# Kernel optimization log

Hardware: AMD Instinct MI355X
Metric: run time of the kernel (lower is better)

Reference implementation:

```python
import jax, jax.numpy as jnp
import numpy as np

N_NODES = 50000
N_EDGES = 800000
N_ENT = 500000
N_REL = 500
L = 2          # num_layers
H = 8          # head_num
D = 16         # per-head dim (hidden_dim // head_num)
HID = H * D    # 128
IN = 128       # in_ent_dim == in_rel_dim == hidden_dim
B = 64         # number of graphs in the batch
SLOPE = 0.2    # leaky-relu negative slope


def setup_inputs() -> dict:
    key = jax.random.key(0)
    ks = jax.random.split(key, 11)
    return {
        "ent_table": jax.random.normal(ks[0], (N_ENT, IN), jnp.float32) * 0.05,
        "rel_table": jax.random.normal(ks[1], (N_REL, IN), jnp.float32) * 0.05,
        "W_ent": jax.random.normal(ks[2], (L, IN, HID), jnp.float32) * 0.05,
        "W_rel": jax.random.normal(ks[3], (L, IN, HID), jnp.float32) * 0.05,
        "attn_l": jax.random.normal(ks[4], (L, H, D), jnp.float32) * 0.05,
        "attn_r": jax.random.normal(ks[5], (L, H, D), jnp.float32) * 0.05,
        "attn_e": jax.random.normal(ks[6], (L, H, D), jnp.float32) * 0.05,
        "ent_ids": jax.random.randint(ks[7], (N_NODES,), 0, N_ENT, jnp.int32),
        "rel_ids": jax.random.randint(ks[8], (N_EDGES,), 0, N_REL, jnp.int32),
        "src": jax.random.randint(ks[9], (N_EDGES,), 0, N_NODES, jnp.int32),
        "dst": jax.random.randint(ks[10], (N_EDGES,), 0, N_NODES, jnp.int32),
        # node-0 offset of each subgraph in the batched graph
        "graph_offsets": jnp.arange(B, dtype=jnp.int32) * (N_NODES // B),
    }


def _kge_layer(h, rel_f, src, dst, W_e, W_r, a_l, a_r, a_e):
    # GAT-style relation-aware message passing (KGELayer)
    feat = (h @ W_e).reshape(-1, H, D)        # [N,H,D]
    rfeat = (rel_f @ W_r).reshape(-1, H, D)   # [E,H,D]
    el = jnp.einsum('nhd,hd->nh', feat, a_l)  # src score
    er = jnp.einsum('nhd,hd->nh', feat, a_r)  # dst score
    ee = jnp.einsum('ehd,hd->eh', rfeat, a_e) # relation score
    e = jax.nn.leaky_relu(el[src] + er[dst] + ee, SLOPE)  # [E,H]
    # segment softmax over incoming edges of each dst node
    emax = jax.ops.segment_max(e, dst, num_segments=N_NODES)
    ex = jnp.exp(e - emax[dst])
    denom = jax.ops.segment_sum(ex, dst, num_segments=N_NODES)
    alpha = ex / denom[dst]                   # [E,H]
    msg = (feat[src] + rfeat) * alpha[:, :, None]  # [E,H,D]
    out = jax.ops.segment_sum(msg, dst, num_segments=N_NODES)  # [N,H,D]
    return out.reshape(-1, HID)


def reference(ent_table, rel_table, W_ent, W_rel, attn_l, attn_r, attn_e,
              ent_ids, rel_ids, src, dst, graph_offsets):
    h = ent_table[ent_ids]       # [N,IN]
    rel_f = rel_table[rel_ids]   # [E,IN]
    for l in range(L):
        h = _kge_layer(h, rel_f, src, dst, W_ent[l], W_rel[l],
                       attn_l[l], attn_r[l], attn_e[l])
    # CLS embedding: node 0 of each unbatched subgraph
    return h[graph_offsets]      # [B,HID]
```

## Files before the change

### kernel.cpp

```cpp
#include <hip/hip_runtime.h>
#include <hip/hip_bf16.h>


#define NN   50000
#define NE   800000
#define NR   500
#define HH   8
#define DD   16
#define HIDD 128
#define BB   64

#define GRIDS 1024
#define PER   784

#define MAXE2 16384
#define MAXS1 16448
#define MAXE1 262144
#define MAXS0 50000


__global__ void k_init(int* slot2, int* slot1, int* slot0, int* counters) {
    int i = blockIdx.x * blockDim.x + threadIdx.x;
    int stride = gridDim.x * blockDim.x;
    for (int n = i; n < NN; n += stride) { slot2[n] = -1; slot1[n] = -1; slot0[n] = -1; }
    if (i < 8) counters[i] = 0;
}

__global__ void k_seed(const int* goffs, int* slot2, int* slot1, int* nodesS1) {
    int i = threadIdx.x;
    if (i < BB) {
        int n = goffs[i];
        slot2[n] = i;
        slot1[n] = -2;
        nodesS1[i] = n;
    }
}

__global__ void k_scan(const int* __restrict__ src, const int* __restrict__ dst,
                       const int* __restrict__ slotHit, int* __restrict__ slotNew,
                       int* eseg, int* ecnt, int* nseg, int* ncnt) {
    __shared__ int cE, cN;
    if (threadIdx.x == 0) { cE = 0; cN = 0; }
    __syncthreads();
    int b = blockIdx.x;
    int lo = b * PER;
    int hi = lo + PER; if (hi > NE) hi = NE;
    int* es = eseg + (size_t)b * PER;
    int* ns = nseg + (size_t)b * PER;
    for (int e = lo + threadIdx.x; e < hi; e += blockDim.x) {
        int d = dst[e];
        if (slotHit[d] >= 0) {
            int pos = atomicAdd(&cE, 1);
            es[pos] = e;
            int s = src[e];
            if (atomicCAS(&slotNew[s], -1, -2) == -1) {
                int p = atomicAdd(&cN, 1);
                ns[p] = s;
            }
        }
    }
    __syncthreads();
    if (threadIdx.x == 0) { ecnt[b] = cE; ncnt[b] = cN; }
}

__device__ int block_scan_counts(const int* cnts, int nblk, int* bases, int offset) {
    __shared__ int part[256];
    __shared__ int total_sh;
    int t = threadIdx.x;
    int per = (nblk + 255) / 256;
    int s = 0;
    for (int j = 0; j < per; j++) { int i = t * per + j; if (i < nblk) s += cnts[i]; }
    part[t] = s;
    __syncthreads();
    for (int d = 1; d < 256; d <<= 1) {
        int v = (t >= d) ? part[t - d] : 0;
        __syncthreads();
        part[t] += v;
        __syncthreads();
    }
    int run = ((t == 0) ? 0 : part[t - 1]) + offset;
    for (int j = 0; j < per; j++) {
        int i = t * per + j;
        if (i < nblk) { bases[i] = run; run += cnts[i]; }
    }
    if (t == 255) total_sh = part[255];
    __syncthreads();
    return total_sh;
}

__global__ void k_prefix2(const int* ecnt2, const int* ncnt2, int* ebase2, int* nbase2,
                          int* counters, const int* nodesS1, int* slot1, int* slot0,
                          int* nodesS0) {
    int t = threadIdx.x;
    int totE = block_scan_counts(ecnt2, GRIDS, ebase2, 0);
    int totN = block_scan_counts(ncnt2, GRIDS, nbase2, BB);
    if (t == 0) {
        counters[2] = totE;
        counters[0] = BB + totN;
        counters[1] = BB + totN;
    }
    if (t < BB) {
        int n = nodesS1[t];
        slot1[n] = t;
        slot0[n] = t;
        nodesS0[t] = n;
    }
}

__global__ void k_compact2(const int* eseg2, const int* ecnt2, const int* ebase2,
                           const int* nseg2, const int* ncnt2, const int* nbase2,
                           int* e2list, int* nodesS1, int* slot1, int* slot0,
                           int* nodesS0, int* deg2) {
    int b = blockIdx.x, t = threadIdx.x;
    int ce = ecnt2[b], cn = ncnt2[b], be = ebase2[b], bn = nbase2[b];
    const int* es = eseg2 + (size_t)b * PER;
    const int* ns = nseg2 + (size_t)b * PER;
    for (int i = t; i < ce; i += blockDim.x) {
        int g = be + i; if (g < MAXE2) e2list[g] = es[i];
    }
    for (int i = t; i < cn; i += blockDim.x) {
        int idx = bn + i;
        if (idx < MAXS1) {
            int n = ns[i];
            nodesS1[idx] = n;
            slot1[n] = idx;
            slot0[n] = idx;
            nodesS0[idx] = n;
        }
    }
    if (b == 0) { for (int i = t; i < BB; i += blockDim.x) deg2[i] = 0; }
}

__global__ void k_prefix1(const int* ecnt1, const int* ncnt1, int* ebase1, int* nbase1,
                          int* counters) {
    int t = threadIdx.x;
    int s0 = counters[1];
    int totE = block_scan_counts(ecnt1, GRIDS, ebase1, 0);
    int totN = block_scan_counts(ncnt1, GRIDS, nbase1, s0);
    if (t == 0) {
        counters[3] = totE;
        counters[1] = s0 + totN;
    }
}

__global__ void k_compact1(const int* eseg1, const int* ecnt1, const int* ebase1,
                           const int* nseg1, const int* ncnt1, const int* nbase1,
                           int* e1list, int* slot0, int* nodesS0,
                           int* deg1, const int* counters) {
    int b = blockIdx.x, t = threadIdx.x;
    int ce = ecnt1[b], cn = ncnt1[b], be = ebase1[b], bn = nbase1[b];
    const int* es = eseg1 + (size_t)b * PER;
    const int* ns = nseg1 + (size_t)b * PER;
    for (int i = t; i < ce; i += blockDim.x) {
        int g = be + i; if (g < MAXE1) e1list[g] = es[i];
    }
    for (int i = t; i < cn; i += blockDim.x) {
        int idx = bn + i;
        if (idx < MAXS0) {
            int n = ns[i];
            slot0[n] = idx;
            nodesS0[idx] = n;
        }
    }
    int cnt1 = counters[0]; if (cnt1 > MAXS1) cnt1 = MAXS1;
    for (int i = b * blockDim.x + t; i < cnt1; i += gridDim.x * blockDim.x) deg1[i] = 0;
}

__global__ void k_hist(const int* e2list, const int* e1list, const int* counters,
                       const int* dst, const int* slot2, const int* slot1,
                       int* deg2, int* deg1) {
    int i = blockIdx.x * blockDim.x + threadIdx.x;
    int stride = gridDim.x * blockDim.x;
    int c2 = counters[2]; if (c2 > MAXE2) c2 = MAXE2;
    int c1 = counters[3]; if (c1 > MAXE1) c1 = MAXE1;
    for (int k = i; k < c2; k += stride) atomicAdd(&deg2[slot2[dst[e2list[k]]]], 1);
    for (int k = i; k < c1; k += stride) atomicAdd(&deg1[slot1[dst[e1list[k]]]], 1);
}

__device__ void excl_scan_glob(const int* deg, int n, int* rp) {
    __shared__ int part[256];
    int t = threadIdx.x;
    int per = (n + 255) / 256;
    int s = 0;
    for (int j = 0; j < per; j++) { int i = t * per + j; if (i < n) s += deg[i]; }
    part[t] = s;
    __syncthreads();
    for (int d = 1; d < 256; d <<= 1) {
        int v = (t >= d) ? part[t - d] : 0;
        __syncthreads();
        part[t] += v;
        __syncthreads();
    }
    int run = (t == 0) ? 0 : part[t - 1];
    for (int j = 0; j < per; j++) {
        int i = t * per + j;
        if (i < n) { rp[i] = run; run += deg[i]; }
    }
    if (t == 255) rp[n] = part[255];
    __syncthreads();
}

__global__ void k_rowptr(const int* deg2, const int* deg1, const int* counters,
                         int* rp2, int* rp1, int* cur2, int* cur1) {
    int t = threadIdx.x;
    int cnt1 = counters[0]; if (cnt1 > MAXS1) cnt1 = MAXS1;
    excl_scan_glob(deg2, BB, rp2);
    excl_scan_glob(deg1, cnt1, rp1);
    for (int i = t; i < BB; i += blockDim.x) cur2[i] = rp2[i];
    for (int i = t; i < cnt1; i += blockDim.x) cur1[i] = rp1[i];
}

__global__ void k_scatter(const int* e2list, const int* e1list, const int* counters,
                          const int* dst, const int* slot2, const int* slot1,
                          int* cur2, int* cur1, int* csr2, int* csr1) {
    int i = blockIdx.x * blockDim.x + threadIdx.x;
    int stride = gridDim.x * blockDim.x;
    int c2 = counters[2]; if (c2 > MAXE2) c2 = MAXE2;
    int c1 = counters[3]; if (c1 > MAXE1) c1 = MAXE1;
    for (int k = i; k < c2; k += stride) {
        int e = e2list[k];
        int pos = atomicAdd(&cur2[slot2[dst[e]]], 1);
        if (pos < MAXE2) csr2[pos] = e;
    }
    for (int k = i; k < c1; k += stride) {
        int e = e1list[k];
        int pos = atomicAdd(&cur1[slot1[dst[e]]], 1);
        if (pos < MAXE1) csr1[pos] = e;
    }
}

#define FT 8
__global__ void k_relfeat0(const float* rel_table, const float* __restrict__ W_rel,
                           const float* attn_e, float* rproj, float* ee,
                           const int* nodesS0, const int* counters, const int* ent_ids,
                           const float* __restrict__ ent_table,
                           const float* __restrict__ W_ent,
                           const float* __restrict__ attn_l,
                           const float* __restrict__ attn_r,
                           float* feat0, float* el0, float* er0) {
    __shared__ float rows[FT][HIDD];
    int t = threadIdx.x;
    if (blockIdx.x < 2 * NR) {
        int l = blockIdx.x / NR, r = blockIdx.x % NR;
        rows[0][t] = rel_table[r * HIDD + t];
        __syncthreads();
        const float* W = W_rel + l * HIDD * HIDD;
        float acc = 0.f;
        for (int j = 0; j < HIDD; j++) acc += rows[0][j] * W[j * HIDD + t];
        rproj[(l * NR + r) * HIDD + t] = acc;
        rows[1][t] = acc;
        __syncthreads();
        if (t < HH) {
            float s = 0.f;
            for (int d = 0; d < DD; d++)
                s += rows[1][t * DD + d] * attn_e[(l * HH + t) * DD + d];
            ee[(l * NR + r) * HH + t] = s;
        }
        return;
    }
    int cnt = counters[1]; if (cnt > MAXS0) cnt = MAXS0;
    int tile0 = blockIdx.x - 2 * NR;
    int tstride = gridDim.x - 2 * NR;
    int nTiles = (cnt + FT - 1) / FT;
    for (int tile = tile0; tile < nTiles; tile += tstride) {
        int k0 = tile * FT;
        #pragma unroll
        for (int m = 0; m < FT; m++) {
            int k = k0 + m;
            int n = nodesS0[k < cnt ? k : 0];
            rows[m][t] = ent_table[(long)ent_ids[n] * HIDD + t];
        }
        __syncthreads();
        float acc[FT];
        #pragma unroll
        for (int m = 0; m < FT; m++) acc[m] = 0.f;
        for (int j = 0; j < HIDD; j++) {
            float w = W_ent[j * HIDD + t];
            #pragma unroll
            for (int m = 0; m < FT; m++) acc[m] += rows[m][j] * w;
        }
        __syncthreads();
        #pragma unroll
        for (int m = 0; m < FT; m++) {
            int k = k0 + m;
            if (k < cnt) feat0[k * HIDD + t] = acc[m];
            rows[m][t] = acc[m];
        }
        __syncthreads();
        {
            int m = t >> 4, idx = t & 15, h = idx >> 1, isR = idx & 1;
            int k = k0 + m;
            if (k < cnt) {
                const float* av = (isR ? attn_r : attn_l) + h * DD;
                float s = 0.f;
                for (int d = 0; d < DD; d++) s += rows[m][h * DD + d] * av[d];
                if (isR) er0[k * HH + h] = s; else el0[k * HH + h] = s;
            }
        }
        __syncthreads();
    }
}

__global__ void k_layer1(const int* counters, const int* rp1, const int* csr1,
                         const int* src, const int* rel_ids, const int* slot0,
                         const float* __restrict__ el0, const float* __restrict__ er0,
                         const float* __restrict__ ee0,
                         const float* __restrict__ feat0, const float* __restrict__ rproj0,
                         const float* __restrict__ W_ent1,
                         const float* attn_l1, const float* attn_r1,
                         float* feat1, float* el1, float* er1) {
    int cnt1 = counters[0]; if (cnt1 > MAXS1) cnt1 = MAXS1;
    int t = threadIdx.x;
    int h = t >> 4;
    __shared__ float row[HIDD];
    __shared__ float f2[HIDD];
    for (int k = blockIdx.x; k < cnt1; k += gridDim.x) {
        int lo = rp1[k], hi = rp1[k + 1];
        float er_k = er0[k * HH + h];
        float acc = 0.f, sumex = 0.f;
        for (int i = lo; i < hi; i++) {
            int e = csr1[i];
            int ks = slot0[src[e]];
            int rid = rel_ids[e];
            float sc = el0[ks * HH + h] + er_k + ee0[rid * HH + h];
            sc = sc >= 0.f ? sc : 0.2f * sc;
            float ex = __expf(sc);
            sumex += ex;
            acc += ex * (feat0[ks * HIDD + t] + rproj0[rid * HIDD + t]);
        }
        row[t] = (hi > lo) ? acc / sumex : 0.f;
        __syncthreads();
        float f = 0.f;
        for (int j = 0; j < HIDD; j++) f += row[j] * W_ent1[j * HIDD + t];
        feat1[k * HIDD + t] = f;
        f2[t] = f;
        __syncthreads();
        if (t < HH) {
            float s = 0.f;
            for (int d = 0; d < DD; d++) s += f2[t * DD + d] * attn_l1[t * DD + d];
            el1[k * HH + t] = s;
        } else if (t < 2 * HH) {
            int hh = t - HH;
            float s = 0.f;
            for (int d = 0; d < DD; d++) s += f2[hh * DD + d] * attn_r1[hh * DD + d];
            er1[k * HH + hh] = s;
        }
        __syncthreads();
    }
}

__global__ void k_layer2(const int* rp2, const int* csr2,
                         const int* src, const int* rel_ids, const int* slot1,
                         const float* __restrict__ el1, const float* __restrict__ er1,
                         const float* __restrict__ ee1,
                         const float* __restrict__ feat1, const float* __restrict__ rproj1,
                         float* out) {
    int g = blockIdx.x;
    int t = threadIdx.x;
    int h = t >> 4;
    int lo = rp2[g], hi = rp2[g + 1];
    float er_g = er1[g * HH + h];
    float acc = 0.f, sumex = 0.f;
    for (int i = lo; i < hi; i++) {
        int e = csr2[i];
        int ks = slot1[src[e]];
        int rid = rel_ids[e];
        float sc = el1[ks * HH + h] + er_g + ee1[rid * HH + h];
        sc = sc >= 0.f ? sc : 0.2f * sc;
        float ex = __expf(sc);
        sumex += ex;
        acc += ex * (feat1[ks * HIDD + t] + rproj1[rid * HIDD + t]);
    }
    out[g * HIDD + t] = (hi > lo) ? acc / sumex : 0.f;
}

extern "C" void kernel_launch(void* const* d_in, const int* in_sizes, int n_in,
                              void* d_out, int out_size, void* d_ws, size_t ws_size,
                              hipStream_t stream) {
    const float* ent_table = (const float*)d_in[0];
    const float* rel_table = (const float*)d_in[1];
    const float* W_ent     = (const float*)d_in[2];
    const float* W_rel     = (const float*)d_in[3];
    const float* attn_l    = (const float*)d_in[4];
    const float* attn_r    = (const float*)d_in[5];
    const float* attn_e    = (const float*)d_in[6];
    const int*   ent_ids   = (const int*)d_in[7];
    const int*   rel_ids   = (const int*)d_in[8];
    const int*   src       = (const int*)d_in[9];
    const int*   dst       = (const int*)d_in[10];
    const int*   goffs     = (const int*)d_in[11];
    float*       out       = (float*)d_out;

    char* p = (char*)d_ws;
    auto alloc = [&](size_t nbytes) {
        void* q = (void*)p;
        p += (nbytes + 255) & ~(size_t)255;
        return q;
    };
    float* rproj   = (float*)alloc((size_t)2 * NR * HIDD * 4);
    float* ee      = (float*)alloc((size_t)2 * NR * HH * 4);
    int*   slot2   = (int*)alloc((size_t)NN * 4);
    int*   slot1   = (int*)alloc((size_t)NN * 4);
    int*   slot0   = (int*)alloc((size_t)NN * 4);
    int*   nodesS1 = (int*)alloc((size_t)MAXS1 * 4);
    int*   nodesS0 = (int*)alloc((size_t)MAXS0 * 4);
    int*   e2list  = (int*)alloc((size_t)MAXE2 * 4);
    int*   e1list  = (int*)alloc((size_t)MAXE1 * 4);
    int*   counters= (int*)alloc(8 * 4);
    int*   eseg2   = (int*)alloc((size_t)GRIDS * PER * 4);
    int*   nseg2   = (int*)alloc((size_t)GRIDS * PER * 4);
    int*   eseg1   = (int*)alloc((size_t)GRIDS * PER * 4);
    int*   nseg1   = (int*)alloc((size_t)GRIDS * PER * 4);
    int*   ecnt2   = (int*)alloc((size_t)GRIDS * 4);
    int*   ncnt2   = (int*)alloc((size_t)GRIDS * 4);
    int*   ecnt1   = (int*)alloc((size_t)GRIDS * 4);
    int*   ncnt1   = (int*)alloc((size_t)GRIDS * 4);
    int*   ebase2  = (int*)alloc((size_t)GRIDS * 4);
    int*   nbase2  = (int*)alloc((size_t)GRIDS * 4);
    int*   ebase1  = (int*)alloc((size_t)GRIDS * 4);
    int*   nbase1  = (int*)alloc((size_t)GRIDS * 4);
    int*   deg2    = (int*)alloc((size_t)BB * 4);
    int*   rp2     = (int*)alloc((size_t)(BB + 1) * 4);
    int*   cur2    = (int*)alloc((size_t)BB * 4);
    int*   deg1    = (int*)alloc((size_t)MAXS1 * 4);
    int*   rp1     = (int*)alloc((size_t)(MAXS1 + 1) * 4);
    int*   cur1    = (int*)alloc((size_t)MAXS1 * 4);
    int*   csr2    = (int*)alloc((size_t)MAXE2 * 4);
    int*   csr1    = (int*)alloc((size_t)MAXE1 * 4);
    float* feat0   = (float*)alloc((size_t)MAXS0 * HIDD * 4);
    float* el0     = (float*)alloc((size_t)MAXS0 * HH * 4);
    float* er0     = (float*)alloc((size_t)MAXS0 * HH * 4);
    float* feat1   = (float*)alloc((size_t)MAXS1 * HIDD * 4);
    float* el1     = (float*)alloc((size_t)MAXS1 * HH * 4);
    float* er1     = (float*)alloc((size_t)MAXS1 * HH * 4);

    const float* rproj0 = rproj;
    const float* rproj1 = rproj + (size_t)NR * HIDD;
    const float* ee0 = ee;
    const float* ee1 = ee + (size_t)NR * HH;
    const float* W_ent0 = W_ent;
    const float* W_ent1 = W_ent + HIDD * HIDD;
    const float* attn_l0 = attn_l, *attn_l1 = attn_l + HH * DD;
    const float* attn_r0 = attn_r, *attn_r1 = attn_r + HH * DD;

    hipLaunchKernelGGL(k_init, dim3(256), dim3(256), 0, stream,
                       slot2, slot1, slot0, counters);
    hipLaunchKernelGGL(k_seed, dim3(1), dim3(64), 0, stream,
                       goffs, slot2, slot1, nodesS1);
    hipLaunchKernelGGL(k_scan, dim3(GRIDS), dim3(256), 0, stream,
                       src, dst, slot2, slot1, eseg2, ecnt2, nseg2, ncnt2);
    hipLaunchKernelGGL(k_prefix2, dim3(1), dim3(256), 0, stream,
                       ecnt2, ncnt2, ebase2, nbase2, counters,
                       nodesS1, slot1, slot0, nodesS0);
    hipLaunchKernelGGL(k_compact2, dim3(GRIDS), dim3(256), 0, stream,
                       eseg2, ecnt2, ebase2, nseg2, ncnt2, nbase2,
                       e2list, nodesS1, slot1, slot0, nodesS0, deg2);
    hipLaunchKernelGGL(k_scan, dim3(GRIDS), dim3(256), 0, stream,
                       src, dst, slot1, slot0, eseg1, ecnt1, nseg1, ncnt1);
    hipLaunchKernelGGL(k_prefix1, dim3(1), dim3(256), 0, stream,
                       ecnt1, ncnt1, ebase1, nbase1, counters);
    hipLaunchKernelGGL(k_compact1, dim3(GRIDS), dim3(256), 0, stream,
                       eseg1, ecnt1, ebase1, nseg1, ncnt1, nbase1,
                       e1list, slot0, nodesS0, deg1, counters);
    hipLaunchKernelGGL(k_hist, dim3(256), dim3(256), 0, stream,
                       e2list, e1list, counters, dst, slot2, slot1, deg2, deg1);
    hipLaunchKernelGGL(k_rowptr, dim3(1), dim3(256), 0, stream,
                       deg2, deg1, counters, rp2, rp1, cur2, cur1);
    hipLaunchKernelGGL(k_scatter, dim3(256), dim3(256), 0, stream,
                       e2list, e1list, counters, dst, slot2, slot1,
                       cur2, cur1, csr2, csr1);
    hipLaunchKernelGGL(k_relfeat0, dim3(2 * NR + 1024), dim3(HIDD), 0, stream,
                       rel_table, W_rel, attn_e, rproj, ee,
                       nodesS0, counters, ent_ids, ent_table, W_ent0,
                       attn_l0, attn_r0, feat0, el0, er0);
    hipLaunchKernelGGL(k_layer1, dim3(2048), dim3(HIDD), 0, stream,
                       counters, rp1, csr1, src, rel_ids, slot0,
                       el0, er0, ee0, feat0, rproj0, W_ent1,
                       attn_l1, attn_r1, feat1, el1, er1);
    hipLaunchKernelGGL(k_layer2, dim3(BB), dim3(HIDD), 0, stream,
                       rp2, csr2, src, rel_ids, slot1,
                       el1, er1, ee1, feat1, rproj1, out);
}
```

Baseline: 436.3 us.

## Fuse degree histogram and CSR scatter into frontier scan and compaction kernels

Restructures the subgraph-extraction preprocessing. Degree counting moves into the scan kernels, the row-pointer scan moves into the prefix kernels, and CSR scattering moves into the compaction kernels, which removes the separate hist, rowptr, scatter and seed launches plus the intermediate edge lists. The hop-2 scan drops the slot2 array and instead binary-searches the 64 sorted graph offsets held in shared memory, and it reads dst as int4. This cuts launch count and global traffic, but relies on graph_offsets being sorted and on NE/PER being multiples of 4 for the vectorised loop.

```diff
diff --git a/kernel.cpp b/kernel.cpp
--- a/kernel.cpp
+++ b/kernel.cpp
@@ -1,5 +1,4 @@
 #include <hip/hip_runtime.h>
-#include <hip/hip_bf16.h>
 
 
 #define NN   50000
@@ -13,59 +12,72 @@
 #define GRIDS 1024
 #define PER   784
 
-#define MAXE2 16384
 #define MAXS1 16448
 #define MAXE1 262144
 #define MAXS0 50000
-
-
-__global__ void k_init(int* slot2, int* slot1, int* slot0, int* counters) {
+#define MAXE2 16384
+
+
+__global__ void k_init(int* slot1, int* slot0, int* counters, int* deg2, int* deg1) {
     int i = blockIdx.x * blockDim.x + threadIdx.x;
     int stride = gridDim.x * blockDim.x;
-    for (int n = i; n < NN; n += stride) { slot2[n] = -1; slot1[n] = -1; slot0[n] = -1; }
+    for (int n = i; n < NN; n += stride) { slot1[n] = -1; slot0[n] = -1; }
+    for (int n = i; n < MAXS1; n += stride) deg1[n] = 0;
+    if (i < BB) deg2[i] = 0;
     if (i < 8) counters[i] = 0;
 }
 
-__global__ void k_seed(const int* goffs, int* slot2, int* slot1, int* nodesS1) {
-    int i = threadIdx.x;
-    if (i < BB) {
-        int n = goffs[i];
-        slot2[n] = i;
-        slot1[n] = -2;
-        nodesS1[i] = n;
-    }
-}
-
-__global__ void k_scan(const int* __restrict__ src, const int* __restrict__ dst,
-                       const int* __restrict__ slotHit, int* __restrict__ slotNew,
-                       int* eseg, int* ecnt, int* nseg, int* ncnt) {
+__global__ void k_scan2(const int* __restrict__ src, const int* __restrict__ dst,
+                        const int* __restrict__ goffs, int* __restrict__ slot1,
+                        int* eseg, int* ecnt, int* nseg, int* ncnt, int* deg2) {
+    __shared__ int sgo[BB];
     __shared__ int cE, cN;
-    if (threadIdx.x == 0) { cE = 0; cN = 0; }
-    __syncthreads();
-    int b = blockIdx.x;
+    int t = threadIdx.x, b = blockIdx.x;
+    if (t < BB) sgo[t] = goffs[t];
+    if (t == 0) { cE = 0; cN = 0; }
+    __syncthreads();
+    auto findg = [&](int d) -> int {
+        int lo = 0, hi = BB - 1;
+        #pragma unroll
+        for (int s = 0; s < 6; s++) {
+            int mid = (lo + hi) >> 1;
+            if (sgo[mid] < d) lo = mid + 1; else hi = mid;
+        }
+        return (sgo[lo] == d) ? lo : -1;
+    };
     int lo = b * PER;
     int hi = lo + PER; if (hi > NE) hi = NE;
-    int* es = eseg + (size_t)b * PER;
-    int* ns = nseg + (size_t)b * PER;
-    for (int e = lo + threadIdx.x; e < hi; e += blockDim.x) {
-        int d = dst[e];
-        if (slotHit[d] >= 0) {
-            int pos = atomicAdd(&cE, 1);
-            es[pos] = e;
-            int s = src[e];
-            if (atomicCAS(&slotNew[s], -1, -2) == -1) {
-                int p = atomicAdd(&cN, 1);
-                ns[p] = s;
+    if (hi > lo) {
+        int* es = eseg + (size_t)b * PER;
+        int* ns = nseg + (size_t)b * PER;
+        const int4* dst4 = (const int4*)(dst + lo);
+        int n4 = (hi - lo) >> 2;
+        for (int q = t; q < n4; q += blockDim.x) {
+            int4 d4 = dst4[q];
+            int eb = lo + q * 4;
+            #pragma unroll
+            for (int c = 0; c < 4; c++) {
+                int d = (&d4.x)[c];
+                int g = findg(d);
+                if (g >= 0) {
+                    int pos = atomicAdd(&cE, 1);
+                    es[pos] = eb + c;
+                    atomicAdd(&deg2[g], 1);
+                    int s = src[eb + c];
+                    if (findg(s) < 0 && atomicCAS(&slot1[s], -1, -2) == -1) {
+                        int pp = atomicAdd(&cN, 1);
+                        ns[pp] = s;
+                    }
+                }
             }
         }
     }
     __syncthreads();
-    if (threadIdx.x == 0) { ecnt[b] = cE; ncnt[b] = cN; }
-}
-
-__device__ int block_scan_counts(const int* cnts, int nblk, int* bases, int offset) {
-    __shared__ int part[256];
-    __shared__ int total_sh;
+    if (t == 0) { ecnt[b] = cE; ncnt[b] = cN; }
+}
+
+__device__ int block_scan_counts(const int* cnts, int nblk, int* bases, int offset,
+                                 int* part) {
     int t = threadIdx.x;
     int per = (nblk + 255) / 256;
     int s = 0;
@@ -83,77 +95,149 @@
         int i = t * per + j;
         if (i < nblk) { bases[i] = run; run += cnts[i]; }
     }
-    if (t == 255) total_sh = part[255];
-    __syncthreads();
-    return total_sh;
-}
-
-__global__ void k_prefix2(const int* ecnt2, const int* ncnt2, int* ebase2, int* nbase2,
-                          int* counters, const int* nodesS1, int* slot1, int* slot0,
-                          int* nodesS0) {
-    int t = threadIdx.x;
-    int totE = block_scan_counts(ecnt2, GRIDS, ebase2, 0);
-    int totN = block_scan_counts(ncnt2, GRIDS, nbase2, BB);
+    int tot = part[255];
+    __syncthreads();
+    return tot;
+}
+
+__device__ void excl_scan_glob(const int* deg, int n, int* rp, int* part) {
+    int t = threadIdx.x;
+    int per = (n + 255) / 256;
+    int s = 0;
+    for (int j = 0; j < per; j++) { int i = t * per + j; if (i < n) s += deg[i]; }
+    part[t] = s;
+    __syncthreads();
+    for (int d = 1; d < 256; d <<= 1) {
+        int v = (t >= d) ? part[t - d] : 0;
+        __syncthreads();
+        part[t] += v;
+        __syncthreads();
+    }
+    int run = (t == 0) ? 0 : part[t - 1];
+    for (int j = 0; j < per; j++) {
+        int i = t * per + j;
+        if (i < n) { rp[i] = run; run += deg[i]; }
+    }
+    if (t == 255) rp[n] = part[255];
+    __syncthreads();
+}
+
+__global__ void k_prefix2(const int* ncnt, int* nbase, int* counters,
+                          const int* goffs, int* slot1, int* slot0, int* nodesS0,
+                          const int* deg2, int* rp2, int* cur2) {
+    __shared__ int part[256];
+    int t = threadIdx.x;
+    int totN = block_scan_counts(ncnt, GRIDS, nbase, BB, part);
     if (t == 0) {
-        counters[2] = totE;
-        counters[0] = BB + totN;
-        counters[1] = BB + totN;
-    }
+        int s1 = BB + totN; if (s1 > MAXS1) s1 = MAXS1;
+        counters[0] = s1;
+        counters[1] = s1;
+    }
+    excl_scan_glob(deg2, BB, rp2, part);
+    for (int i = t; i < BB; i += blockDim.x) cur2[i] = rp2[i];
     if (t < BB) {
-        int n = nodesS1[t];
+        int n = goffs[t];
         slot1[n] = t;
         slot0[n] = t;
         nodesS0[t] = n;
     }
 }
 
-__global__ void k_compact2(const int* eseg2, const int* ecnt2, const int* ebase2,
-                           const int* nseg2, const int* ncnt2, const int* nbase2,
-                           int* e2list, int* nodesS1, int* slot1, int* slot0,
-                           int* nodesS0, int* deg2) {
-    int b = blockIdx.x, t = threadIdx.x;
-    int ce = ecnt2[b], cn = ncnt2[b], be = ebase2[b], bn = nbase2[b];
-    const int* es = eseg2 + (size_t)b * PER;
-    const int* ns = nseg2 + (size_t)b * PER;
-    for (int i = t; i < ce; i += blockDim.x) {
-        int g = be + i; if (g < MAXE2) e2list[g] = es[i];
-    }
+__global__ void k_compact2(const int* eseg, const int* ecnt,
+                           const int* nseg, const int* ncnt, const int* nbase,
+                           const int* goffs, const int* dst,
+                           int* slot1, int* slot0, int* nodesS0,
+                           int* cur2, int* csr2) {
+    __shared__ int sgo[BB];
+    int t = threadIdx.x, b = blockIdx.x;
+    if (t < BB) sgo[t] = goffs[t];
+    __syncthreads();
+    int ce = ecnt[b], cn = ncnt[b], bn = nbase[b];
+    const int* es = eseg + (size_t)b * PER;
+    const int* ns = nseg + (size_t)b * PER;
     for (int i = t; i < cn; i += blockDim.x) {
         int idx = bn + i;
         if (idx < MAXS1) {
             int n = ns[i];
-            nodesS1[idx] = n;
             slot1[n] = idx;
             slot0[n] = idx;
             nodesS0[idx] = n;
         }
     }
-    if (b == 0) { for (int i = t; i < BB; i += blockDim.x) deg2[i] = 0; }
-}
-
-__global__ void k_prefix1(const int* ecnt1, const int* ncnt1, int* ebase1, int* nbase1,
-                          int* counters) {
+    for (int i = t; i < ce; i += blockDim.x) {
+        int e = es[i];
+        int d = dst[e];
+        int lo = 0, hi = BB - 1;
+        #pragma unroll
+        for (int s = 0; s < 6; s++) {
+            int mid = (lo + hi) >> 1;
+            if (sgo[mid] < d) lo = mid + 1; else hi = mid;
+        }
+        int pos = atomicAdd(&cur2[lo], 1);
+        if (pos < MAXE2) csr2[pos] = e;
+    }
+}
+
+__global__ void k_scan1(const int* __restrict__ src, const int* __restrict__ dst,
+                        const int* __restrict__ slot1, int* __restrict__ slot0,
+                        int* eseg, int* ecnt, int* nseg, int* ncnt, int* deg1) {
+    __shared__ int cE, cN;
+    int t = threadIdx.x, b = blockIdx.x;
+    if (t == 0) { cE = 0; cN = 0; }
+    __syncthreads();
+    int lo = b * PER;
+    int hi = lo + PER; if (hi > NE) hi = NE;
+    if (hi > lo) {
+        int* es = eseg + (size_t)b * PER;
+        int* ns = nseg + (size_t)b * PER;
+        const int4* dst4 = (const int4*)(dst + lo);
+        int n4 = (hi - lo) >> 2;
+        for (int q = t; q < n4; q += blockDim.x) {
+            int4 d4 = dst4[q];
+            int eb = lo + q * 4;
+            #pragma unroll
+            for (int c = 0; c < 4; c++) {
+                int kd = slot1[(&d4.x)[c]];
+                if (kd >= 0) {
+                    int pos = atomicAdd(&cE, 1);
+                    es[pos] = eb + c;
+                    atomicAdd(&deg1[kd], 1);
+                    int s = src[eb + c];
+                    if (atomicCAS(&slot0[s], -1, -2) == -1) {
+                        int pp = atomicAdd(&cN, 1);
+                        ns[pp] = s;
+                    }
+                }
+            }
+        }
+    }
+    __syncthreads();
+    if (t == 0) { ecnt[b] = cE; ncnt[b] = cN; }
+}
+
+__global__ void k_prefix1(const int* ncnt, int* nbase, int* counters,
+                          const int* deg1, int* rp1, int* cur1) {
+    __shared__ int part[256];
     int t = threadIdx.x;
     int s0 = counters[1];
-    int totE = block_scan_counts(ecnt1, GRIDS, ebase1, 0);
-    int totN = block_scan_counts(ncnt1, GRIDS, nbase1, s0);
+    int cnt1 = counters[0];
+    int totN = block_scan_counts(ncnt, GRIDS, nbase, s0, part);
     if (t == 0) {
-        counters[3] = totE;
-        counters[1] = s0 + totN;
-    }
-}
-
-__global__ void k_compact1(const int* eseg1, const int* ecnt1, const int* ebase1,
-                           const int* nseg1, const int* ncnt1, const int* nbase1,
-                           int* e1list, int* slot0, int* nodesS0,
-                           int* deg1, const int* counters) {
-    int b = blockIdx.x, t = threadIdx.x;
-    int ce = ecnt1[b], cn = ncnt1[b], be = ebase1[b], bn = nbase1[b];
-    const int* es = eseg1 + (size_t)b * PER;
-    const int* ns = nseg1 + (size_t)b * PER;
-    for (int i = t; i < ce; i += blockDim.x) {
-        int g = be + i; if (g < MAXE1) e1list[g] = es[i];
-    }
+        int v = s0 + totN; if (v > MAXS0) v = MAXS0;
+        counters[1] = v;
+    }
+    excl_scan_glob(deg1, cnt1, rp1, part);
+    for (int i = t; i < cnt1; i += blockDim.x) cur1[i] = rp1[i];
+}
+
+__global__ void k_compact1(const int* eseg, const int* ecnt,
+                           const int* nseg, const int* ncnt, const int* nbase,
+                           const int* dst, const int* slot1,
+                           int* slot0, int* nodesS0, int* cur1, int* csr1) {
+    int t = threadIdx.x, b = blockIdx.x;
+    int ce = ecnt[b], cn = ncnt[b], bn = nbase[b];
+    const int* es = eseg + (size_t)b * PER;
+    const int* ns = nseg + (size_t)b * PER;
     for (int i = t; i < cn; i += blockDim.x) {
         int idx = bn + i;
         if (idx < MAXS0) {
@@ -162,69 +246,10 @@
             nodesS0[idx] = n;
         }
     }
-    int cnt1 = counters[0]; if (cnt1 > MAXS1) cnt1 = MAXS1;
-    for (int i = b * blockDim.x + t; i < cnt1; i += gridDim.x * blockDim.x) deg1[i] = 0;
-}
-
-__global__ void k_hist(const int* e2list, const int* e1list, const int* counters,
-                       const int* dst, const int* slot2, const int* slot1,
-                       int* deg2, int* deg1) {
-    int i = blockIdx.x * blockDim.x + threadIdx.x;
-    int stride = gridDim.x * blockDim.x;
-    int c2 = counters[2]; if (c2 > MAXE2) c2 = MAXE2;
-    int c1 = counters[3]; if (c1 > MAXE1) c1 = MAXE1;
-    for (int k = i; k < c2; k += stride) atomicAdd(&deg2[slot2[dst[e2list[k]]]], 1);
-    for (int k = i; k < c1; k += stride) atomicAdd(&deg1[slot1[dst[e1list[k]]]], 1);
-}
-
-__device__ void excl_scan_glob(const int* deg, int n, int* rp) {
-    __shared__ int part[256];
-    int t = threadIdx.x;
-    int per = (n + 255) / 256;
-    int s = 0;
-    for (int j = 0; j < per; j++) { int i = t * per + j; if (i < n) s += deg[i]; }
-    part[t] = s;
-    __syncthreads();
-    for (int d = 1; d < 256; d <<= 1) {
-        int v = (t >= d) ? part[t - d] : 0;
-        __syncthreads();
-        part[t] += v;
-        __syncthreads();
-    }
-    int run = (t == 0) ? 0 : part[t - 1];
-    for (int j = 0; j < per; j++) {
-        int i = t * per + j;
-        if (i < n) { rp[i] = run; run += deg[i]; }
-    }
-    if (t == 255) rp[n] = part[255];
-    __syncthreads();
-}
-
-__global__ void k_rowptr(const int* deg2, const int* deg1, const int* counters,
-                         int* rp2, int* rp1, int* cur2, int* cur1) {
-    int t = threadIdx.x;
-    int cnt1 = counters[0]; if (cnt1 > MAXS1) cnt1 = MAXS1;
-    excl_scan_glob(deg2, BB, rp2);
-    excl_scan_glob(deg1, cnt1, rp1);
-    for (int i = t; i < BB; i += blockDim.x) cur2[i] = rp2[i];
-    for (int i = t; i < cnt1; i += blockDim.x) cur1[i] = rp1[i];
-}
-
-__global__ void k_scatter(const int* e2list, const int* e1list, const int* counters,
-                          const int* dst, const int* slot2, const int* slot1,
-                          int* cur2, int* cur1, int* csr2, int* csr1) {
-    int i = blockIdx.x * blockDim.x + threadIdx.x;
-    int stride = gridDim.x * blockDim.x;
-    int c2 = counters[2]; if (c2 > MAXE2) c2 = MAXE2;
-    int c1 = counters[3]; if (c1 > MAXE1) c1 = MAXE1;
-    for (int k = i; k < c2; k += stride) {
-        int e = e2list[k];
-        int pos = atomicAdd(&cur2[slot2[dst[e]]], 1);
-        if (pos < MAXE2) csr2[pos] = e;
-    }
-    for (int k = i; k < c1; k += stride) {
-        int e = e1list[k];
-        int pos = atomicAdd(&cur1[slot1[dst[e]]], 1);
+    for (int i = t; i < ce; i += blockDim.x) {
+        int e = es[i];
+        int kd = slot1[dst[e]];
+        int pos = atomicAdd(&cur1[kd], 1);
         if (pos < MAXE1) csr1[pos] = e;
     }
 }
@@ -268,7 +293,7 @@
         for (int m = 0; m < FT; m++) {
             int k = k0 + m;
             int n = nodesS0[k < cnt ? k : 0];
-            rows[m][t] = ent_table[(long)ent_ids[n] * HIDD + t];
+            rows[m][t] = ent_table[(size_t)ent_ids[n] * HIDD + t];
         }
         __syncthreads();
         float acc[FT];
@@ -283,7 +308,7 @@
         #pragma unroll
         for (int m = 0; m < FT; m++) {
             int k = k0 + m;
-            if (k < cnt) feat0[k * HIDD + t] = acc[m];
+            if (k < cnt) feat0[(size_t)k * HIDD + t] = acc[m];
             rows[m][t] = acc[m];
         }
         __syncthreads();
@@ -309,7 +334,7 @@
                          const float* __restrict__ W_ent1,
                          const float* attn_l1, const float* attn_r1,
                          float* feat1, float* el1, float* er1) {
-    int cnt1 = counters[0]; if (cnt1 > MAXS1) cnt1 = MAXS1;
+    int cnt1 = counters[0];
     int t = threadIdx.x;
     int h = t >> 4;
     __shared__ float row[HIDD];
@@ -326,13 +351,13 @@
             sc = sc >= 0.f ? sc : 0.2f * sc;
             float ex = __expf(sc);
             sumex += ex;
-            acc += ex * (feat0[ks * HIDD + t] + rproj0[rid * HIDD + t]);
+            acc += ex * (feat0[(size_t)ks * HIDD + t] + rproj0[rid * HIDD + t]);
         }
         row[t] = (hi > lo) ? acc / sumex : 0.f;
         __syncthreads();
         float f = 0.f;
         for (int j = 0; j < HIDD; j++) f += row[j] * W_ent1[j * HIDD + t];
-        feat1[k * HIDD + t] = f;
+        feat1[(size_t)k * HIDD + t] = f;
         f2[t] = f;
         __syncthreads();
         if (t < HH) {
@@ -369,7 +394,7 @@
         sc = sc >= 0.f ? sc : 0.2f * sc;
         float ex = __expf(sc);
         sumex += ex;
-        acc += ex * (feat1[ks * HIDD + t] + rproj1[rid * HIDD + t]);
+        acc += ex * (feat1[(size_t)ks * HIDD + t] + rproj1[rid * HIDD + t]);
     }
     out[g * HIDD + t] = (hi > lo) ? acc / sumex : 0.f;
 }
@@ -399,26 +424,15 @@
     };
     float* rproj   = (float*)alloc((size_t)2 * NR * HIDD * 4);
     float* ee      = (float*)alloc((size_t)2 * NR * HH * 4);
-    int*   slot2   = (int*)alloc((size_t)NN * 4);
     int*   slot1   = (int*)alloc((size_t)NN * 4);
     int*   slot0   = (int*)alloc((size_t)NN * 4);
-    int*   nodesS1 = (int*)alloc((size_t)MAXS1 * 4);
     int*   nodesS0 = (int*)alloc((size_t)MAXS0 * 4);
-    int*   e2list  = (int*)alloc((size_t)MAXE2 * 4);
-    int*   e1list  = (int*)alloc((size_t)MAXE1 * 4);
     int*   counters= (int*)alloc(8 * 4);
-    int*   eseg2   = (int*)alloc((size_t)GRIDS * PER * 4);
-    int*   nseg2   = (int*)alloc((size_t)GRIDS * PER * 4);
-    int*   eseg1   = (int*)alloc((size_t)GRIDS * PER * 4);
-    int*   nseg1   = (int*)alloc((size_t)GRIDS * PER * 4);
-    int*   ecnt2   = (int*)alloc((size_t)GRIDS * 4);
-    int*   ncnt2   = (int*)alloc((size_t)GRIDS * 4);
-    int*   ecnt1   = (int*)alloc((size_t)GRIDS * 4);
-    int*   ncnt1   = (int*)alloc((size_t)GRIDS * 4);
-    int*   ebase2  = (int*)alloc((size_t)GRIDS * 4);
-    int*   nbase2  = (int*)alloc((size_t)GRIDS * 4);
-    int*   ebase1  = (int*)alloc((size_t)GRIDS * 4);
-    int*   nbase1  = (int*)alloc((size_t)GRIDS * 4);
+    int*   eseg    = (int*)alloc((size_t)GRIDS * PER * 4);
+    int*   nseg    = (int*)alloc((size_t)GRIDS * PER * 4);
+    int*   ecnt    = (int*)alloc((size_t)GRIDS * 4);
+    int*   ncnt    = (int*)alloc((size_t)GRIDS * 4);
+    int*   nbase   = (int*)alloc((size_t)GRIDS * 4);
     int*   deg2    = (int*)alloc((size_t)BB * 4);
     int*   rp2     = (int*)alloc((size_t)(BB + 1) * 4);
     int*   cur2    = (int*)alloc((size_t)BB * 4);
@@ -444,31 +458,22 @@
     const float* attn_r0 = attn_r, *attn_r1 = attn_r + HH * DD;
 
     hipLaunchKernelGGL(k_init, dim3(256), dim3(256), 0, stream,
-                       slot2, slot1, slot0, counters);
-    hipLaunchKernelGGL(k_seed, dim3(1), dim3(64), 0, stream,
-                       goffs, slot2, slot1, nodesS1);
-    hipLaunchKernelGGL(k_scan, dim3(GRIDS), dim3(256), 0, stream,
-                       src, dst, slot2, slot1, eseg2, ecnt2, nseg2, ncnt2);
+                       slot1, slot0, counters, deg2, deg1);
+    hipLaunchKernelGGL(k_scan2, dim3(GRIDS), dim3(256), 0, stream,
+                       src, dst, goffs, slot1, eseg, ecnt, nseg, ncnt, deg2);
     hipLaunchKernelGGL(k_prefix2, dim3(1), dim3(256), 0, stream,
-                       ecnt2, ncnt2, ebase2, nbase2, counters,
-                       nodesS1, slot1, slot0, nodesS0);
+                       ncnt, nbase, counters, goffs, slot1, slot0, nodesS0,
+                       deg2, rp2, cur2);
     hipLaunchKernelGGL(k_compact2, dim3(GRIDS), dim3(256), 0, stream,
-                       eseg2, ecnt2, ebase2, nseg2, ncnt2, nbase2,
-                       e2list, nodesS1, slot1, slot0, nodesS0, deg2);
-    hipLaunchKernelGGL(k_scan, dim3(GRIDS), dim3(256), 0, stream,
-                       src, dst, slot1, slot0, eseg1, ecnt1, nseg1, ncnt1);
+                       eseg, ecnt, nseg, ncnt, nbase, goffs, dst,
+                       slot1, slot0, nodesS0, cur2, csr2);
+    hipLaunchKernelGGL(k_scan1, dim3(GRIDS), dim3(256), 0, stream,
+                       src, dst, slot1, slot0, eseg, ecnt, nseg, ncnt, deg1);
     hipLaunchKernelGGL(k_prefix1, dim3(1), dim3(256), 0, stream,
-                       ecnt1, ncnt1, ebase1, nbase1, counters);
+                       ncnt, nbase, counters, deg1, rp1, cur1);
     hipLaunchKernelGGL(k_compact1, dim3(GRIDS), dim3(256), 0, stream,
-                       eseg1, ecnt1, ebase1, nseg1, ncnt1, nbase1,
-                       e1list, slot0, nodesS0, deg1, counters);
-    hipLaunchKernelGGL(k_hist, dim3(256), dim3(256), 0, stream,
-                       e2list, e1list, counters, dst, slot2, slot1, deg2, deg1);
-    hipLaunchKernelGGL(k_rowptr, dim3(1), dim3(256), 0, stream,
-                       deg2, deg1, counters, rp2, rp1, cur2, cur1);
-    hipLaunchKernelGGL(k_scatter, dim3(256), dim3(256), 0, stream,
-                       e2list, e1list, counters, dst, slot2, slot1,
-                       cur2, cur1, csr2, csr1);
+                       eseg, ecnt, nseg, ncnt, nbase, dst, slot1,
+                       slot0, nodesS0, cur1, csr1);
     hipLaunchKernelGGL(k_relfeat0, dim3(2 * NR + 1024), dim3(HIDD), 0, stream,
                        rel_table, W_rel, attn_e, rproj, ee,
                        nodesS0, counters, ent_ids, ent_table, W_ent0,
```

Result: no change. 429.9 us (-1.5%).
